# Kernel tuning notes

Measured on AMD Instinct MI355X. Metric: run time of the kernel, lower is better.

Reference implementation:

```python
import jax, jax.numpy as jnp
import numpy as np

FEAT_STRIDE = 16
SCALES = np.array([8.0, 16.0, 32.0], np.float32)
RATIOS = np.array([0.5, 1.0, 2.0], np.float32)
PRE_NMS = 6000
POST_NMS = 300
NMS_THRESH = 0.7
MIN_SIZE = 16.0


def _base_anchors():
    bs = float(FEAT_STRIDE)
    ctr = (bs - 1.0) * 0.5
    size = bs * bs
    ws = np.round(np.sqrt(size / RATIOS))
    hs = np.round(ws * RATIOS)
    anchors = []
    for w, h in zip(ws, hs):
        for s in SCALES:
            ww, hh = w * s, h * s
            anchors.append([ctr - 0.5 * (ww - 1), ctr - 0.5 * (hh - 1),
                            ctr + 0.5 * (ww - 1), ctr + 0.5 * (hh - 1)])
    return np.array(anchors, np.float32)  # [A=9, 4]


def _all_anchors(H, W):
    base = _base_anchors()
    sx = np.arange(W, dtype=np.float32) * FEAT_STRIDE
    sy = np.arange(H, dtype=np.float32) * FEAT_STRIDE
    gx, gy = np.meshgrid(sx, sy)  # [H, W]
    shifts = np.stack([gx.ravel(), gy.ravel(), gx.ravel(), gy.ravel()], axis=1)  # [H*W, 4]
    return jnp.asarray((shifts[:, None, :] + base[None, :, :]).reshape(-1, 4))  # [H*W*A, 4]


def _conv2d(x, w, b, pad):
    y = jax.lax.conv_general_dilated(x, w, (1, 1), pad,
                                     dimension_numbers=('NCHW', 'OIHW', 'NCHW'))
    return y + b[None, :, None, None]


def _decode(anchors, deltas):
    wa = anchors[:, 2] - anchors[:, 0] + 1.0
    ha = anchors[:, 3] - anchors[:, 1] + 1.0
    cxa = anchors[:, 0] + 0.5 * wa
    cya = anchors[:, 1] + 0.5 * ha
    cx = deltas[:, 0] * wa + cxa
    cy = deltas[:, 1] * ha + cya
    w = wa * jnp.exp(deltas[:, 2])
    h = ha * jnp.exp(deltas[:, 3])
    return jnp.stack([cx - 0.5 * w, cy - 0.5 * h, cx + 0.5 * w, cy + 0.5 * h], axis=1)


def _pairwise_iou(b):
    x1, y1, x2, y2 = b[:, 0], b[:, 1], b[:, 2], b[:, 3]
    areas = (x2 - x1 + 1.0) * (y2 - y1 + 1.0)
    iw = jnp.clip(jnp.minimum(x2[:, None], x2[None, :]) - jnp.maximum(x1[:, None], x1[None, :]) + 1.0, 0.0)
    ih = jnp.clip(jnp.minimum(y2[:, None], y2[None, :]) - jnp.maximum(y1[:, None], y1[None, :]) + 1.0, 0.0)
    inter = iw * ih
    return inter / (areas[:, None] + areas[None, :] - inter)


def _proposal(bbox_pred, scores, anchors, im_info):
    boxes = _decode(anchors, bbox_pred)
    x1 = jnp.clip(boxes[:, 0], 0.0, im_info[1] - 1.0)
    y1 = jnp.clip(boxes[:, 1], 0.0, im_info[0] - 1.0)
    x2 = jnp.clip(boxes[:, 2], 0.0, im_info[1] - 1.0)
    y2 = jnp.clip(boxes[:, 3], 0.0, im_info[0] - 1.0)
    boxes = jnp.stack([x1, y1, x2, y2], axis=1)
    min_sz = MIN_SIZE * im_info[2]
    valid = ((x2 - x1 + 1.0) >= min_sz) & ((y2 - y1 + 1.0) >= min_sz)
    sc = jnp.where(valid, scores, -1.0)
    top_sc, idx = jax.lax.top_k(sc, PRE_NMS)
    props = boxes[idx]  # [PRE_NMS, 4], score-descending
    iou = _pairwise_iou(props)

    def body(i, keep):
        sup = (iou[i] > NMS_THRESH) & keep[i]
        return keep & ~(sup & (jnp.arange(PRE_NMS) > i))

    keep = jax.lax.fori_loop(0, PRE_NMS, body, jnp.ones((PRE_NMS,), bool))
    keep = keep & (top_sc > 0.0)
    order = jnp.argsort(jnp.logical_not(keep), stable=True)  # kept first, score order preserved
    sel = order[:POST_NMS]
    mask = (jnp.arange(POST_NMS) < jnp.sum(keep))[:, None]
    return jnp.where(mask, props[sel], 0.0)


def setup_inputs() -> dict:
    key = jax.random.key(0)
    ks = jax.random.split(key, 4)
    feature_map = jax.random.normal(ks[0], (1, 1024, 84, 125), jnp.float32)
    im_info = jnp.array([1344.0, 2000.0, 1.0], jnp.float32)  # (H, W, scale)
    conv_w = jax.random.normal(ks[1], (512, 1024, 3, 3), jnp.float32) * 0.01
    conv_b = jnp.zeros((512,), jnp.float32)
    cls_w = jax.random.normal(ks[2], (18, 512, 1, 1), jnp.float32) * 0.01
    cls_b = jnp.zeros((18,), jnp.float32)
    reg_w = jax.random.normal(ks[3], (36, 512, 1, 1), jnp.float32) * 0.01
    reg_b = jnp.zeros((36,), jnp.float32)
    return {"feature_map": feature_map, "im_info": im_info, "conv_w": conv_w,
            "conv_b": conv_b, "cls_w": cls_w, "cls_b": cls_b, "reg_w": reg_w, "reg_b": reg_b}


def reference(feature_map, im_info, conv_w, conv_b, cls_w, cls_b, reg_w, reg_b):
    B, C, H, W = feature_map.shape
    anchors = _all_anchors(H, W)  # [H*W*9, 4]
    fm = jax.nn.relu(_conv2d(feature_map, conv_w, conv_b, [(1, 1), (1, 1)]))
    cls = _conv2d(fm, cls_w, cls_b, [(0, 0), (0, 0)])  # [B, 18, H, W]
    reg = _conv2d(fm, reg_w, reg_b, [(0, 0), (0, 0)])  # [B, 36, H, W]
    cls_scores = cls.transpose(0, 2, 3, 1).reshape(-1, 2)
    bbox_pred = reg.transpose(0, 2, 3, 1).reshape(-1, 4)
    fg_probs = jax.nn.softmax(jax.lax.stop_gradient(cls_scores), axis=1)[:, 1]
    rois = _proposal(bbox_pred, fg_probs, anchors, im_info)
    return (bbox_pred, cls_scores, rois, anchors)
```

## Files before the change

### kernel.cpp

```cpp
#include <hip/hip_runtime.h>

typedef unsigned int u32;
typedef unsigned long long u64;

#define H_ 84
#define W_ 125
#define CIN 1024
#define CMID 512
#define NPOS 10500
#define NA 94500
#define PRE 6000
#define POST 300
#define FMROW 128
#define FMSTRIDE 10752
#define SELCAP 16384

__constant__ float c_aw[9] = {184.f, 368.f, 736.f, 128.f, 256.f, 512.f, 88.f, 176.f, 352.f};
__constant__ float c_ah[9] = { 96.f, 192.f, 384.f, 128.f, 256.f, 512.f, 176.f, 352.f, 704.f};

#define OFF_FM      0ull
#define OFF_BOXES   22020096ull
#define OFF_KEYS    23532096ull
#define OFF_SELA    24288096ull
#define OFF_SELB    24419168ull
#define OFF_PROPS   24550240ull
#define OFF_AREAS   24646240ull
#define OFF_VALIDW  24670240ull
#define OFF_MASK    24671008ull
#define OFF_KEEPW   29279008ull

__global__ __launch_bounds__(256, 4) void k_conv3(const float* __restrict__ in,
                                                  const float* __restrict__ w,
                                                  const float* __restrict__ bias,
                                                  float* __restrict__ fm) {
  __shared__ float Xs[16 * 4 * 132];
  const int tid = threadIdx.x;
  const int lane = tid & 63;
  const int wvi = __builtin_amdgcn_readfirstlane(tid >> 6);
  const int ocb = blockIdx.x;
  const int y0 = blockIdx.y * 2;
  const int oc0 = ocb * 16 + wvi * 4;

  float acc[4][2][2];
#pragma unroll
  for (int o = 0; o < 4; ++o)
#pragma unroll
    for (int r = 0; r < 2; ++r) {
      acc[o][r][0] = 0.f;
      acc[o][r][1] = 0.f;
    }

  const int cb = 2 * lane;

#pragma unroll 1
  for (int icb = 0; icb < CIN; icb += 16) {
    __syncthreads();
#pragma unroll
    for (int k = 0; k < 33; ++k) {
      int l = tid + k * 256;
      int r132 = l / 132;
      int c = l - r132 * 132;
      int i = r132 >> 2;
      int rr = r132 & 3;
      int yi = y0 - 1 + rr;
      int xi = c - 1;
      float v = 0.f;
      if ((unsigned)yi < 84u && (unsigned)xi < 125u)
        v = in[(icb + i) * (H_ * W_) + yi * W_ + xi];
      Xs[l] = v;
    }
    __syncthreads();

#pragma unroll 2
    for (int i = 0; i < 16; ++i) {
      const int ic = icb + i;
      float ws[4][9];
#pragma unroll
      for (int o = 0; o < 4; ++o)
#pragma unroll
        for (int e = 0; e < 9; ++e)
          ws[o][e] = w[(oc0 + o) * 9216 + ic * 9 + e];

      float x4[4][4];
#pragma unroll
      for (int rr = 0; rr < 4; ++rr) {
        float2 lo = *(const float2*)&Xs[(i * 4 + rr) * 132 + cb];
        float2 hi = *(const float2*)&Xs[(i * 4 + rr) * 132 + cb + 2];
        x4[rr][0] = lo.x;
        x4[rr][1] = lo.y;
        x4[rr][2] = hi.x;
        x4[rr][3] = hi.y;
      }

#pragma unroll
      for (int o = 0; o < 4; ++o)
#pragma unroll
        for (int r = 0; r < 2; ++r)
#pragma unroll
          for (int ky = 0; ky < 3; ++ky)
#pragma unroll
            for (int kx = 0; kx < 3; ++kx) {
              float wv2 = ws[o][ky * 3 + kx];
              acc[o][r][0] += wv2 * x4[r + ky][kx];
              acc[o][r][1] += wv2 * x4[r + ky][kx + 1];
            }
    }
  }

  const int px = 2 * lane;
#pragma unroll
  for (int o = 0; o < 4; ++o) {
    float b = bias[oc0 + o];
#pragma unroll
    for (int r = 0; r < 2; ++r) {
      float2 v;
      v.x = fmaxf(acc[o][r][0] + b, 0.f);
      v.y = fmaxf(acc[o][r][1] + b, 0.f);
      *(float2*)&fm[(oc0 + o) * FMSTRIDE + (y0 + r) * FMROW + px] = v;
    }
  }
}

__global__ __launch_bounds__(64) void k_heads(const float* __restrict__ fm,
                                              const float* __restrict__ cls_w,
                                              const float* __restrict__ cls_b,
                                              const float* __restrict__ reg_w,
                                              const float* __restrict__ reg_b,
                                              const float* __restrict__ iminfo,
                                              float* __restrict__ out_bbox,
                                              float* __restrict__ out_cls,
                                              float* __restrict__ out_anch,
                                              float* __restrict__ boxes,
                                              uint2* __restrict__ keys) {
  __shared__ float wl[64 * 56];
  const int tid = threadIdx.x;
  const int p = blockIdx.x * 64 + tid;
  const int pc = p < NPOS ? p : NPOS - 1;
  const int py = pc / W_;
  const int px = pc % W_;
  const int pos = py * FMROW + px;

  float acc[56];
#pragma unroll
  for (int o = 0; o < 56; ++o) acc[o] = 0.f;

#pragma unroll 1
  for (int icb = 0; icb < CMID; icb += 64) {
    __syncthreads();
    for (int l = tid; l < 64 * 54; l += 64) {
      int ic = l / 54;
      int o = l % 54;
      float wv = (o < 18) ? cls_w[o * CMID + icb + ic] : reg_w[(o - 18) * CMID + icb + ic];
      wl[ic * 56 + o] = wv;
    }
    __syncthreads();
#pragma unroll 4
    for (int i = 0; i < 64; ++i) {
      float v = fm[(icb + i) * FMSTRIDE + pos];
#pragma unroll
      for (int o4 = 0; o4 < 14; ++o4) {
        float4 w4 = *(const float4*)&wl[i * 56 + o4 * 4];
        acc[o4 * 4 + 0] += w4.x * v;
        acc[o4 * 4 + 1] += w4.y * v;
        acc[o4 * 4 + 2] += w4.z * v;
        acc[o4 * 4 + 3] += w4.w * v;
      }
    }
  }
  if (p >= NPOS) return;

  const float imh = iminfo[0];
  const float imw = iminfo[1];
  const float minsz = 16.0f * iminfo[2];

#pragma unroll
  for (int a = 0; a < 9; ++a) {
    const int n = p * 9 + a;
    float s0 = acc[a * 2 + 0] + cls_b[a * 2 + 0];
    float s1 = acc[a * 2 + 1] + cls_b[a * 2 + 1];
    out_cls[n * 2 + 0] = s0;
    out_cls[n * 2 + 1] = s1;

    float dx = acc[18 + a * 4 + 0] + reg_b[a * 4 + 0];
    float dy = acc[18 + a * 4 + 1] + reg_b[a * 4 + 1];
    float dw = acc[18 + a * 4 + 2] + reg_b[a * 4 + 2];
    float dh = acc[18 + a * 4 + 3] + reg_b[a * 4 + 3];
    out_bbox[n * 4 + 0] = dx;
    out_bbox[n * 4 + 1] = dy;
    out_bbox[n * 4 + 2] = dw;
    out_bbox[n * 4 + 3] = dh;

    float aw = c_aw[a], ah = c_ah[a];
    float cxs = px * 16.0f + 7.5f;
    float cys = py * 16.0f + 7.5f;
    float ax1 = cxs - 0.5f * (aw - 1.0f);
    float ay1 = cys - 0.5f * (ah - 1.0f);
    float ax2 = cxs + 0.5f * (aw - 1.0f);
    float ay2 = cys + 0.5f * (ah - 1.0f);
    out_anch[n * 4 + 0] = ax1;
    out_anch[n * 4 + 1] = ay1;
    out_anch[n * 4 + 2] = ax2;
    out_anch[n * 4 + 3] = ay2;

    float wa = ax2 - ax1 + 1.0f;
    float ha = ay2 - ay1 + 1.0f;
    float cxa = ax1 + 0.5f * wa;
    float cya = ay1 + 0.5f * ha;
    float cx = dx * wa + cxa;
    float cy = dy * ha + cya;
    float ww = wa * expf(dw);
    float hh = ha * expf(dh);
    float bx1 = cx - 0.5f * ww;
    float by1 = cy - 0.5f * hh;
    float bx2 = cx + 0.5f * ww;
    float by2 = cy + 0.5f * hh;
    bx1 = fminf(fmaxf(bx1, 0.f), imw - 1.f);
    by1 = fminf(fmaxf(by1, 0.f), imh - 1.f);
    bx2 = fminf(fmaxf(bx2, 0.f), imw - 1.f);
    by2 = fminf(fmaxf(by2, 0.f), imh - 1.f);
    boxes[n * 4 + 0] = bx1;
    boxes[n * 4 + 1] = by1;
    boxes[n * 4 + 2] = bx2;
    boxes[n * 4 + 3] = by2;

    bool valid = (bx2 - bx1 + 1.0f >= minsz) && (by2 - by1 + 1.0f >= minsz);
    float prob = 1.0f / (1.0f + expf(s0 - s1));
    u32 key = valid ? __float_as_uint(prob) : 0u;
    keys[n] = make_uint2(~key, (u32)n);
  }
}

__global__ __launch_bounds__(512) void k_select(const uint2* __restrict__ keys,
                                                uint2* __restrict__ selA,
                                                uint2* __restrict__ selB) {
  __shared__ u32 h[8192];
  __shared__ u32 stot[512];
  __shared__ u32 sB1, sLt1, sB2, sN;
  const int t = threadIdx.x;
  const int s = t * 185;
  const int e = (s + 185 < NA) ? s + 185 : NA;

  for (int i = t; i < 4096; i += 512) h[i] = 0;
  __syncthreads();
  for (int i = s; i < e; ++i) atomicAdd(&h[keys[i].x >> 20], 1u);
  __syncthreads();
  {
    u32 loc = 0;
#pragma unroll
    for (int j = 0; j < 8; ++j) loc += h[t * 8 + j];
    stot[t] = loc;
    __syncthreads();
    for (int off = 1; off < 512; off <<= 1) {
      u32 add = (t >= off) ? stot[t - off] : 0u;
      __syncthreads();
      stot[t] += add;
      __syncthreads();
    }
    u32 cb = stot[t] - loc;
    if (cb < PRE && stot[t] >= PRE) {
      u32 run = cb;
#pragma unroll
      for (int j = 0; j < 8; ++j) {
        u32 c = h[t * 8 + j];
        if (run < PRE && run + c >= PRE) { sB1 = t * 8 + j; sLt1 = run; }
        run += c;
      }
    }
  }
  __syncthreads();
  const u32 B1 = sB1;
  const u32 T2 = PRE - sLt1;

  for (int i = t; i < 4096; i += 512) h[i] = 0;
  __syncthreads();
  for (int i = s; i < e; ++i) {
    u32 k = keys[i].x;
    if ((k >> 20) == B1) atomicAdd(&h[(k >> 8) & 0xFFFu], 1u);
  }
  __syncthreads();
  {
    u32 loc = 0;
#pragma unroll
    for (int j = 0; j < 8; ++j) loc += h[t * 8 + j];
    stot[t] = loc;
    __syncthreads();
    for (int off = 1; off < 512; off <<= 1) {
      u32 add = (t >= off) ? stot[t - off] : 0u;
      __syncthreads();
      stot[t] += add;
      __syncthreads();
    }
    u32 cb = stot[t] - loc;
    if (cb < T2 && stot[t] >= T2) {
      u32 run = cb;
#pragma unroll
      for (int j = 0; j < 8; ++j) {
        u32 c = h[t * 8 + j];
        if (run < T2 && run + c >= T2) { sB2 = t * 8 + j; }
        run += c;
      }
    }
  }
  __syncthreads();
  const u32 B2 = sB2;

  u32 cnt = 0;
  for (int i = s; i < e; ++i) {
    u32 k = keys[i].x;
    u32 hi = k >> 20;
    if (hi < B1 || (hi == B1 && ((k >> 8) & 0xFFFu) <= B2)) cnt++;
  }
  stot[t] = cnt;
  __syncthreads();
  for (int off = 1; off < 512; off <<= 1) {
    u32 add = (t >= off) ? stot[t - off] : 0u;
    __syncthreads();
    stot[t] += add;
    __syncthreads();
  }
  u32 base = stot[t] - cnt;
  if (t == 511) sN = stot[511] < SELCAP ? stot[511] : SELCAP;
  for (int i = s; i < e; ++i) {
    uint2 v = keys[i];
    u32 hi = v.x >> 20;
    if (hi < B1 || (hi == B1 && ((v.x >> 8) & 0xFFFu) <= B2)) {
      if (base < SELCAP) selA[base] = v;
      base++;
    }
  }
  __syncthreads();
  const int n = (int)sN;

  const int q = (n + 511) / 512;
  const int s2 = t * q;
  const int e2 = (s2 + q < n) ? s2 + q : n;
  uint2* src = selA;
  uint2* dst = selB;
#pragma unroll 1
  for (int pass = 0; pass < 8; ++pass) {
    const int sh = pass * 4;
#pragma unroll
    for (int k = 0; k < 16; ++k) h[k * 512 + t] = 0;
    __syncthreads();
    for (int i = s2; i < e2; ++i) {
      u32 d = (src[i].x >> sh) & 15u;
      h[d * 512 + t] += 1;
    }
    __syncthreads();
    u32 run = 0;
#pragma unroll
    for (int j = 0; j < 16; ++j) {
      u32 v = h[t * 16 + j];
      h[t * 16 + j] = run;
      run += v;
    }
    stot[t] = run;
    __syncthreads();
    for (int off = 1; off < 512; off <<= 1) {
      u32 add = (t >= off) ? stot[t - off] : 0u;
      __syncthreads();
      stot[t] += add;
      __syncthreads();
    }
    u32 cb = (t > 0) ? stot[t - 1] : 0u;
#pragma unroll
    for (int j = 0; j < 16; ++j) h[t * 16 + j] += cb;
    __syncthreads();
    for (int i = s2; i < e2; ++i) {
      uint2 v = src[i];
      u32 d = (v.x >> sh) & 15u;
      u32 off = h[d * 512 + t];
      h[d * 512 + t] = off + 1;
      dst[off] = v;
    }
    __syncthreads();
    uint2* tmp = src;
    src = dst;
    dst = tmp;
  }
}

__global__ __launch_bounds__(256) void k_gather(const uint2* __restrict__ sel,
                                                const float4* __restrict__ boxes,
                                                float4* __restrict__ props,
                                                float* __restrict__ areas,
                                                u64* __restrict__ validw) {
  const int k = blockIdx.x * 256 + threadIdx.x;
  bool valid = false;
  if (k < PRE) {
    uint2 kv = sel[k];
    u32 key = ~kv.x;
    valid = key > 0u;
    float4 b = boxes[kv.y];
    props[k] = b;
    areas[k] = (b.z - b.x + 1.0f) * (b.w - b.y + 1.0f);
  }
  u64 bal = __ballot(valid);
  if ((threadIdx.x & 63) == 0 && k < PRE) validw[k >> 6] = bal;
}

__global__ __launch_bounds__(256) void k_iou(const float4* __restrict__ props,
                                             const float* __restrict__ areas,
                                             u64* __restrict__ mask) {
  const int gid = blockIdx.x * 256 + threadIdx.x;
  const int i = gid / 94;
  const int w = gid - i * 94;
  if (i >= PRE) return;
  u64 bits = 0;
  const int j0 = w * 64;
  if (j0 + 63 > i) {
    float4 bi = props[i];
    float ai = areas[i];
    for (int b = 0; b < 64; ++b) {
      int j = j0 + b;
      if (j > i && j < PRE) {
        float4 bj = props[j];
        float iw = fminf(bi.z, bj.z) - fmaxf(bi.x, bj.x) + 1.0f;
        float ih = fminf(bi.w, bj.w) - fmaxf(bi.y, bj.y) + 1.0f;
        iw = fmaxf(iw, 0.f);
        ih = fmaxf(ih, 0.f);
        float inter = iw * ih;
        float aj = areas[j];
        if (inter > 0.7f * (ai + aj - inter)) bits |= (1ull << b);
      }
    }
  }
  mask[(u64)i * 96 + w] = bits;
}

__device__ __forceinline__ u64 bcast_u64(u64 v, int src) {
  u32 lo = (u32)v;
  u32 hi = (u32)(v >> 32);
  lo = (u32)__shfl((int)lo, src, 64);
  hi = (u32)__shfl((int)hi, src, 64);
  return ((u64)hi << 32) | (u64)lo;
}

__global__ __launch_bounds__(64) void k_nms(const u64* __restrict__ mask,
                                            const u64* __restrict__ validw,
                                            u64* __restrict__ keepw) {
  const int lane = threadIdx.x;
  const int w0 = (2 * lane < 96) ? 2 * lane : 0;
  const int w1 = (2 * lane < 96) ? 2 * lane + 1 : 1;
  u64 s0 = 0, s1 = 0;
  u64 b0[16], b1[16];
#pragma unroll
  for (int d = 0; d < 16; ++d) {
    b0[d] = mask[(u64)d * 96 + w0];
    b1[d] = mask[(u64)d * 96 + w1];
  }
#pragma unroll 1
  for (int i0 = 0; i0 < PRE; i0 += 16) {
#pragma unroll
    for (int d = 0; d < 16; ++d) {
      int i = i0 + d;
      int w = i >> 6;
      u64 cand = (w & 1) ? s1 : s0;
      u64 word = bcast_u64(cand, w >> 1);
      bool sup = (word >> (i & 63)) & 1ull;
      if (!sup) {
        s0 |= b0[d];
        s1 |= b1[d];
      }
      int ip = i + 16;
      if (ip > PRE - 1) ip = PRE - 1;
      b0[d] = mask[(u64)ip * 96 + w0];
      b1[d] = mask[(u64)ip * 96 + w1];
    }
  }
  if (2 * lane < 94) keepw[2 * lane] = ~s0 & validw[2 * lane];
  if (2 * lane + 1 < 94) keepw[2 * lane + 1] = ~s1 & validw[2 * lane + 1];
}

__global__ __launch_bounds__(128) void k_emit(const u64* __restrict__ keepw,
                                              const float4* __restrict__ props,
                                              float* __restrict__ rois) {
  __shared__ u32 base[94];
  const int t = threadIdx.x;
  for (int r = t; r < POST * 4; r += 128) rois[r] = 0.f;
  if (t < 94) base[t] = (u32)__popcll(keepw[t]);
  __syncthreads();
  if (t == 0) {
    u32 run = 0;
    for (int q = 0; q < 94; ++q) {
      u32 c = base[q];
      base[q] = run;
      run += c;
    }
  }
  __syncthreads();
  if (t < 94) {
    u64 kw = keepw[t];
    int rank = (int)base[t];
    while (kw) {
      int b = __ffsll((unsigned long long)kw) - 1;
      kw &= kw - 1;
      if (rank < POST) {
        float4 v = props[t * 64 + b];
        rois[rank * 4 + 0] = v.x;
        rois[rank * 4 + 1] = v.y;
        rois[rank * 4 + 2] = v.z;
        rois[rank * 4 + 3] = v.w;
      }
      rank++;
    }
  }
}

extern "C" void kernel_launch(void* const* d_in, const int* in_sizes, int n_in,
                              void* d_out, int out_size, void* d_ws, size_t ws_size,
                              hipStream_t stream) {
  const float* feat   = (const float*)d_in[0];
  const float* iminfo = (const float*)d_in[1];
  const float* conv_w = (const float*)d_in[2];
  const float* conv_b = (const float*)d_in[3];
  const float* cls_w  = (const float*)d_in[4];
  const float* cls_b  = (const float*)d_in[5];
  const float* reg_w  = (const float*)d_in[6];
  const float* reg_b  = (const float*)d_in[7];

  float* out = (float*)d_out;
  float* out_bbox = out;
  float* out_cls  = out + 378000;
  float* out_rois = out + 567000;
  float* out_anch = out + 568200;

  char* ws = (char*)d_ws;
  float* fm      = (float*)(ws + OFF_FM);
  float* boxes   = (float*)(ws + OFF_BOXES);
  uint2* keysA   = (uint2*)(ws + OFF_KEYS);
  uint2* selA    = (uint2*)(ws + OFF_SELA);
  uint2* selB    = (uint2*)(ws + OFF_SELB);
  float4* props  = (float4*)(ws + OFF_PROPS);
  float* areas   = (float*)(ws + OFF_AREAS);
  u64* validw    = (u64*)(ws + OFF_VALIDW);
  u64* mask      = (u64*)(ws + OFF_MASK);
  u64* keepw     = (u64*)(ws + OFF_KEEPW);

  k_conv3<<<dim3(32, 42), 256, 0, stream>>>(feat, conv_w, conv_b, fm);
  k_heads<<<165, 64, 0, stream>>>(fm, cls_w, cls_b, reg_w, reg_b, iminfo,
                                  out_bbox, out_cls, out_anch, boxes, keysA);
  k_select<<<1, 512, 0, stream>>>(keysA, selA, selB);
  k_gather<<<24, 256, 0, stream>>>(selA, (const float4*)boxes, props, areas, validw);
  k_iou<<<2204, 256, 0, stream>>>(props, areas, mask);
  k_nms<<<1, 64, 0, stream>>>(mask, validw, keepw);
  k_emit<<<1, 128, 0, stream>>>(keepw, props, out_rois);
}
```

Baseline: 3.078 ms.

## Prefetch next conv input tile into registers and stage IoU boxes in LDS

The 3x3 conv kernel now loads the next 16-channel input tile into a 33-entry register buffer while the current tile is being computed, so the global-load latency overlaps with the FMA work instead of stalling between barriers. The IoU kernel is remapped to a 2D grid where each block shares one 64-wide column of boxes staged in shared memory, which replaces repeated per-thread global loads of the same boxes. In exchange the conv kernel uses more registers, which may lower occupancy, and IoU blocks whose rows all sit below the diagonal still pay for the shared-memory staging.

```diff
diff --git a/kernel.cpp b/kernel.cpp
--- a/kernel.cpp
+++ b/kernel.cpp
@@ -52,24 +52,44 @@
 
   const int cb = 2 * lane;
 
+  float rbuf[33];
+#pragma unroll
+  for (int k = 0; k < 33; ++k) {
+    const int l = tid + k * 256;
+    const int r132 = l / 132;
+    const int c = l - r132 * 132;
+    const int i = r132 >> 2;
+    const int rr = r132 & 3;
+    const int yi = y0 - 1 + rr;
+    const int xi = c - 1;
+    float v = 0.f;
+    if ((unsigned)yi < 84u && (unsigned)xi < 125u)
+      v = in[i * (H_ * W_) + yi * W_ + xi];
+    rbuf[k] = v;
+  }
+
 #pragma unroll 1
   for (int icb = 0; icb < CIN; icb += 16) {
     __syncthreads();
 #pragma unroll
+    for (int k = 0; k < 33; ++k) Xs[tid + k * 256] = rbuf[k];
+    __syncthreads();
+
+    const int icb2 = (icb + 16 < CIN) ? icb + 16 : icb;
+#pragma unroll
     for (int k = 0; k < 33; ++k) {
-      int l = tid + k * 256;
-      int r132 = l / 132;
-      int c = l - r132 * 132;
-      int i = r132 >> 2;
-      int rr = r132 & 3;
-      int yi = y0 - 1 + rr;
-      int xi = c - 1;
+      const int l = tid + k * 256;
+      const int r132 = l / 132;
+      const int c = l - r132 * 132;
+      const int i = r132 >> 2;
+      const int rr = r132 & 3;
+      const int yi = y0 - 1 + rr;
+      const int xi = c - 1;
       float v = 0.f;
       if ((unsigned)yi < 84u && (unsigned)xi < 125u)
-        v = in[(icb + i) * (H_ * W_) + yi * W_ + xi];
-      Xs[l] = v;
-    }
-    __syncthreads();
+        v = in[(icb2 + i) * (H_ * W_) + yi * W_ + xi];
+      rbuf[k] = v;
+    }
 
 #pragma unroll 2
     for (int i = 0; i < 16; ++i) {
@@ -402,30 +422,39 @@
 __global__ __launch_bounds__(256) void k_iou(const float4* __restrict__ props,
                                              const float* __restrict__ areas,
                                              u64* __restrict__ mask) {
-  const int gid = blockIdx.x * 256 + threadIdx.x;
-  const int i = gid / 94;
-  const int w = gid - i * 94;
+  __shared__ float4 pj[64];
+  __shared__ float aj[64];
+  const int t = threadIdx.x;
+  const int jw = blockIdx.x;
+  const int i = blockIdx.y * 256 + t;
+  if (t < 64) {
+    const int jj = jw * 64 + t;
+    float4 z = {0.f, 0.f, 0.f, 0.f};
+    pj[t] = (jj < PRE) ? props[jj] : z;
+    aj[t] = (jj < PRE) ? areas[jj] : 0.f;
+  }
+  __syncthreads();
   if (i >= PRE) return;
+  const int j0 = jw * 64;
   u64 bits = 0;
-  const int j0 = w * 64;
   if (j0 + 63 > i) {
-    float4 bi = props[i];
-    float ai = areas[i];
+    const float4 bi = props[i];
+    const float ai = areas[i];
+#pragma unroll 8
     for (int b = 0; b < 64; ++b) {
-      int j = j0 + b;
+      const int j = j0 + b;
       if (j > i && j < PRE) {
-        float4 bj = props[j];
+        float4 bj = pj[b];
         float iw = fminf(bi.z, bj.z) - fmaxf(bi.x, bj.x) + 1.0f;
         float ih = fminf(bi.w, bj.w) - fmaxf(bi.y, bj.y) + 1.0f;
         iw = fmaxf(iw, 0.f);
         ih = fmaxf(ih, 0.f);
         float inter = iw * ih;
-        float aj = areas[j];
-        if (inter > 0.7f * (ai + aj - inter)) bits |= (1ull << b);
-      }
-    }
-  }
-  mask[(u64)i * 96 + w] = bits;
+        if (inter > 0.7f * (ai + aj[b] - inter)) bits |= (1ull << b);
+      }
+    }
+  }
+  mask[(u64)i * 96 + jw] = bits;
 }
 
 __device__ __forceinline__ u64 bcast_u64(u64 v, int src) {
@@ -542,7 +571,7 @@
                                   out_bbox, out_cls, out_anch, boxes, keysA);
   k_select<<<1, 512, 0, stream>>>(keysA, selA, selB);
   k_gather<<<24, 256, 0, stream>>>(selA, (const float4*)boxes, props, areas, validw);
-  k_iou<<<2204, 256, 0, stream>>>(props, areas, mask);
+  k_iou<<<dim3(94, 24), 256, 0, stream>>>(props, areas, mask);
   k_nms<<<1, 64, 0, stream>>>(mask, validw, keepw);
   k_emit<<<1, 128, 0, stream>>>(keepw, props, out_rois);
 }
```

New measurement: 3.261 ms. 1.06x slower.
